# Performance work log

Hardware: AMD Instinct MI355X
Metric: run time of the kernel (lower is better)

## Reference

```python
import jax, jax.numpy as jnp
import numpy as np

N_NODES = 50000
N_EDGES = 800000
F_IN = 128
HID = 64
N_LAYERS = 3
N_GRAPHS = 64
N_CLASS = 2


def setup_inputs() -> dict:
    key = jax.random.key(0)
    ks = jax.random.split(key, 8)
    x = jax.random.normal(ks[0], (N_NODES, F_IN), jnp.float32)
    edge_index = jax.random.randint(ks[1], (2, N_EDGES), 0, N_NODES, dtype=jnp.int32)
    # sorted, balanced graph assignment so every graph id appears (max-pool safe)
    batch = (jnp.arange(N_NODES, dtype=jnp.int32) * N_GRAPHS) // N_NODES

    def lin(k, fi, fo):
        return jax.random.normal(k, (fi, fo), jnp.float32) / np.sqrt(fi).astype(np.float32)

    W1 = lin(ks[2], F_IN, HID)
    W2 = lin(ks[3], HID, HID)
    W3 = lin(ks[4], HID, HID)
    lin1_W = lin(ks[5], 3 * N_LAYERS * HID, HID)
    lin2_W = lin(ks[6], HID, N_CLASS)
    return dict(
        x=x,
        W1=W1, b1=jnp.zeros((HID,), jnp.float32),
        W2=W2, b2=jnp.zeros((HID,), jnp.float32),
        W3=W3, b3=jnp.zeros((HID,), jnp.float32),
        lin1_W=lin1_W, lin1_b=jnp.zeros((HID,), jnp.float32),
        lin2_W=lin2_W, lin2_b=jnp.zeros((N_CLASS,), jnp.float32),
        edge_index=edge_index, batch=batch,
    )


def reference(x, W1, b1, W2, b2, W3, b3, lin1_W, lin1_b, lin2_W, lin2_b,
              edge_index, batch):
    src, dst = edge_index[0], edge_index[1]
    # GCN symmetric normalization with self-loops (computed once, shared by layers)
    deg = jax.ops.segment_sum(jnp.ones((N_EDGES,), jnp.float32), dst, N_NODES) + 1.0
    dinv = jax.lax.rsqrt(deg)                      # [N]
    enorm = dinv[src] * dinv[dst]                  # [E]
    self_norm = (dinv * dinv)[:, None]             # [N,1] self-loop coeff

    def gcn_conv(h, W, b):
        h = h @ W                                  # [N, HID]
        agg = jax.ops.segment_sum(h[src] * enorm[:, None], dst, N_NODES)
        return agg + self_norm * h + b

    h = jax.nn.relu(gcn_conv(x, W1, b1))
    xs = [h]
    for W, b in ((W2, b2), (W3, b3)):
        h = jax.nn.relu(gcn_conv(h, W, b))
        xs.append(h)
    hcat = jnp.concatenate(xs, axis=1)             # JK 'cat': [N, 3*HID]

    add = jax.ops.segment_sum(hcat, batch, N_GRAPHS)
    cnt = jax.ops.segment_sum(jnp.ones((N_NODES,), jnp.float32), batch, N_GRAPHS)
    mean = add / cnt[:, None]
    mx = jax.ops.segment_max(hcat, batch, N_GRAPHS)
    g = jnp.concatenate([add, mean, mx], axis=1)   # [G, 9*HID]

    g = jax.nn.relu(g @ lin1_W + lin1_b)
    # dropout p=0.5 is identity in eval mode
    logits = g @ lin2_W + lin2_b
    return jax.nn.log_softmax(logits, axis=-1)
```

## Files before the change

### kernel.cpp

```cpp
#include <hip/hip_runtime.h>
#include <hip/hip_fp16.h>

#define N_NODES 50000
#define N_EDGES 800000
#define F_IN 128
#define HID 64
#define N_GRAPHS 64

#define SCAN_B ((N_NODES + 255) / 256)
#define FUSE_B ((N_EDGES + 255) / 256)

typedef _Float16 half8 __attribute__((ext_vector_type(8)));
typedef float f32x4 __attribute__((ext_vector_type(4)));

__global__ void deg_kernel(const int* __restrict__ ei, int* __restrict__ ideg, int E) {
    int i = blockIdx.x * blockDim.x + threadIdx.x;
    if (i * 4 >= E) return;
    int4 d = ((const int4*)(ei + E))[i];
    atomicAdd(&ideg[d.x], 1);
    atomicAdd(&ideg[d.y], 1);
    atomicAdd(&ideg[d.z], 1);
    atomicAdd(&ideg[d.w], 1);
}

__global__ void scan_part(const int* __restrict__ ideg, int* __restrict__ bsum, int n) {
    __shared__ int s[256];
    int t = threadIdx.x;
    int i = blockIdx.x * 256 + t;
    s[t] = (i < n) ? ideg[i] : 0;
    __syncthreads();
    for (int o = 128; o > 0; o >>= 1) {
        if (t < o) s[t] += s[t + o];
        __syncthreads();
    }
    if (t == 0) bsum[blockIdx.x] = s[0];
}

__global__ void scan_base(const int* __restrict__ bsum, int* __restrict__ bbase, int B) {
    __shared__ int s[256];
    int t = threadIdx.x;
    s[t] = (t < B) ? bsum[t] : 0;
    __syncthreads();
    for (int o = 1; o < 256; o <<= 1) {
        int v = (t >= o) ? s[t - o] : 0;
        __syncthreads();
        s[t] += v;
        __syncthreads();
    }
    if (t < B) bbase[t] = (t == 0) ? 0 : s[t - 1];
}

__global__ void scan_final(const int* __restrict__ ideg, const int* __restrict__ bbase,
                           int* __restrict__ offs, int* __restrict__ cur,
                           float* __restrict__ dinv, int n) {
    __shared__ int s[256];
    int t = threadIdx.x;
    int i = blockIdx.x * 256 + t;
    int v = (i < n) ? ideg[i] : 0;
    s[t] = v;
    __syncthreads();
    for (int o = 1; o < 256; o <<= 1) {
        int u = (t >= o) ? s[t - o] : 0;
        __syncthreads();
        s[t] += u;
        __syncthreads();
    }
    int excl = bbase[blockIdx.x] + s[t] - v;
    if (i < n) {
        offs[i] = excl; cur[i] = excl;
        dinv[i] = rsqrtf((float)v + 1.0f);
    }
    if (i == n - 1) offs[n] = excl + v;
}

__global__ void pack_weights(const float* __restrict__ W1, const float* __restrict__ W2,
                             const float* __restrict__ W3,
                             __half* __restrict__ W1t, __half* __restrict__ W2t,
                             __half* __restrict__ W3t) {
    int i = blockIdx.x * 256 + threadIdx.x;
    if (i < 8192) {
        int f = i >> 7, k = i & 127;
        W1t[i] = __float2half(W1[k * 64 + f]);
    } else if (i < 12288) {
        int j = i - 8192;
        int f = j >> 6, k = j & 63;
        W2t[j] = __float2half(W2[k * 64 + f]);
    } else if (i < 16384) {
        int l = i - 12288;
        int f = l >> 6, k = l & 63;
        W3t[l] = __float2half(W3[k * 64 + f]);
    }
}

__global__ __launch_bounds__(256) void fused_fill_mm1(
        const int* __restrict__ ei, const float* __restrict__ dinv,
        int* __restrict__ cur, unsigned int* __restrict__ csr,
        const float* __restrict__ X, const __half* __restrict__ W1t,
        __half* __restrict__ Y16, int E) {
    constexpr int SX = 136;
    __shared__ __half sXh[16 * SX];
    int tid = threadIdx.x;

    int e = blockIdx.x * 256 + tid;
    int esrc = ei[e];
    int d = ei[E + e];
    __half hw = __float2half(dinv[esrc]);
    unsigned int pk = ((unsigned int)(*(unsigned short*)&hw) << 16)
                    | (unsigned int)(esrc & 0xFFFF);
    int pos = atomicAdd(&cur[d], 1);

    int lane = tid & 63;
    int r = lane & 15, h = lane >> 4;
    int w = tid >> 6;
    const half8* Brow = (const half8*)(W1t + (size_t)(w * 16 + r) * F_IN + h * 8);
    half8 b0 = Brow[0];
    half8 b1 = Brow[4];
    half8 b2 = Brow[8];
    half8 b3 = Brow[12];

    int nodeBase = blockIdx.x * 16;
#pragma unroll
    for (int p = tid; p < 512; p += 256) {
        int row = p >> 5, c4 = p & 31;
        float4 v = *(const float4*)(X + (size_t)(nodeBase + row) * F_IN + c4 * 4);
        __half2 ab = __floats2half2_rn(v.x, v.y);
        __half2 cd = __floats2half2_rn(v.z, v.w);
        uint2 u; u.x = *(unsigned int*)&ab; u.y = *(unsigned int*)&cd;
        *(uint2*)&sXh[row * SX + c4 * 4] = u;
    }
    __syncthreads();

    f32x4 acc = {0.f, 0.f, 0.f, 0.f};
    half8 a0 = *(const half8*)&sXh[r * SX +  0 + h * 8];
    half8 a1 = *(const half8*)&sXh[r * SX + 32 + h * 8];
    half8 a2 = *(const half8*)&sXh[r * SX + 64 + h * 8];
    half8 a3 = *(const half8*)&sXh[r * SX + 96 + h * 8];
    acc = __builtin_amdgcn_mfma_f32_16x16x32_f16(a0, b0, acc, 0, 0, 0);
    acc = __builtin_amdgcn_mfma_f32_16x16x32_f16(a1, b1, acc, 0, 0, 0);
    acc = __builtin_amdgcn_mfma_f32_16x16x32_f16(a2, b2, acc, 0, 0, 0);
    acc = __builtin_amdgcn_mfma_f32_16x16x32_f16(a3, b3, acc, 0, 0, 0);
    int nodeT = nodeBase + h * 4;
#pragma unroll
    for (int reg = 0; reg < 4; ++reg)
        Y16[(size_t)(nodeT + reg) * 64 + w * 16 + r] = __float2half(acc[reg]);

    csr[pos] = pk;
}

__global__ __launch_bounds__(256) void matmul64_h(
        const __half* __restrict__ X, const __half* __restrict__ Wt,
        __half* __restrict__ Y16, int n) {
    int tid = threadIdx.x;
    int nodeBase = blockIdx.x * 64;
    int lane = tid & 63;
    int r = lane & 15, h = lane >> 4;
    int w = tid >> 6;
    int rowA = nodeBase + w * 16 + r;
    const half8* Arow = (const half8*)(X + (size_t)rowA * 64 + h * 8);
    half8 a0 = Arow[0];
    half8 a1 = Arow[4];
#pragma unroll
    for (int ft = 0; ft < 4; ++ft) {
        const half8* Brow = (const half8*)(Wt + (size_t)(ft * 16 + r) * 64 + h * 8);
        half8 b0 = Brow[0];
        half8 b1 = Brow[4];
        f32x4 acc = {0.f, 0.f, 0.f, 0.f};
        acc = __builtin_amdgcn_mfma_f32_16x16x32_f16(a0, b0, acc, 0, 0, 0);
        acc = __builtin_amdgcn_mfma_f32_16x16x32_f16(a1, b1, acc, 0, 0, 0);
        int nodeT = nodeBase + w * 16 + h * 4;
#pragma unroll
        for (int reg = 0; reg < 4; ++reg) {
            int node = nodeT + reg;
            if (node < n) Y16[(size_t)node * 64 + ft * 16 + r] = __float2half(acc[reg]);
        }
    }
}

__global__ void agg_kernel(const __half* __restrict__ hp16, const float* __restrict__ dinv,
                           const int* __restrict__ offs, const unsigned int* __restrict__ csr,
                           const float* __restrict__ b, __half* __restrict__ hout, int n) {
    int node = blockIdx.x * 4 + (threadIdx.x >> 6);
    if (node >= n) return;
    int lane = threadIdx.x & 63;
    int g = lane >> 3;
    int sub = lane & 7;
    int beg = offs[node], end = offs[node + 1];

    float a0 = 0.f, a1 = 0.f, a2 = 0.f, a3 = 0.f;
    float a4 = 0.f, a5 = 0.f, a6 = 0.f, a7 = 0.f;
#pragma unroll 2
    for (int i = beg; i < end; i += 8) {
        int idx = i + g;
        unsigned int pk = csr[min(idx, end - 1)];
        int src = (int)(pk & 0xFFFFu);
        __half_raw hr; hr.x = (unsigned short)(pk >> 16);
        float w = (idx < end) ? __half2float(*(__half*)&hr) : 0.f;
        uint4 hv = *(const uint4*)(hp16 + (size_t)src * 64 + sub * 8);
        float2 f01 = __half22float2(*(const __half2*)&hv.x);
        float2 f23 = __half22float2(*(const __half2*)&hv.y);
        float2 f45 = __half22float2(*(const __half2*)&hv.z);
        float2 f67 = __half22float2(*(const __half2*)&hv.w);
        a0 += f01.x * w; a1 += f01.y * w; a2 += f23.x * w; a3 += f23.y * w;
        a4 += f45.x * w; a5 += f45.y * w; a6 += f67.x * w; a7 += f67.y * w;
    }
#pragma unroll
    for (int m = 8; m <= 32; m <<= 1) {
        a0 += __shfl_xor(a0, m); a1 += __shfl_xor(a1, m);
        a2 += __shfl_xor(a2, m); a3 += __shfl_xor(a3, m);
        a4 += __shfl_xor(a4, m); a5 += __shfl_xor(a5, m);
        a6 += __shfl_xor(a6, m); a7 += __shfl_xor(a7, m);
    }

    float dn = dinv[node];
    uint4 sv = *(const uint4*)(hp16 + (size_t)node * 64 + sub * 8);
    float2 s01 = __half22float2(*(const __half2*)&sv.x);
    float2 s23 = __half22float2(*(const __half2*)&sv.y);
    float2 s45 = __half22float2(*(const __half2*)&sv.z);
    float2 s67 = __half22float2(*(const __half2*)&sv.w);
    float4 bA = *(const float4*)(b + sub * 8);
    float4 bB = *(const float4*)(b + sub * 8 + 4);
    float dn2 = dn * dn;
    float4 rA, rB;
    rA.x = dn * a0 + dn2 * s01.x + bA.x;  rA.x = rA.x > 0.f ? rA.x : 0.f;
    rA.y = dn * a1 + dn2 * s01.y + bA.y;  rA.y = rA.y > 0.f ? rA.y : 0.f;
    rA.z = dn * a2 + dn2 * s23.x + bA.z;  rA.z = rA.z > 0.f ? rA.z : 0.f;
    rA.w = dn * a3 + dn2 * s23.y + bA.w;  rA.w = rA.w > 0.f ? rA.w : 0.f;
    rB.x = dn * a4 + dn2 * s45.x + bB.x;  rB.x = rB.x > 0.f ? rB.x : 0.f;
    rB.y = dn * a5 + dn2 * s45.y + bB.y;  rB.y = rB.y > 0.f ? rB.y : 0.f;
    rB.z = dn * a6 + dn2 * s67.x + bB.z;  rB.z = rB.z > 0.f ? rB.z : 0.f;
    rB.w = dn * a7 + dn2 * s67.y + bB.w;  rB.w = rB.w > 0.f ? rB.w : 0.f;
    if (g == 0) {
        __half2 p0 = __floats2half2_rn(rA.x, rA.y);
        __half2 p1 = __floats2half2_rn(rA.z, rA.w);
        __half2 p2 = __floats2half2_rn(rB.x, rB.y);
        __half2 p3 = __floats2half2_rn(rB.z, rB.w);
        uint4 st;
        st.x = *(unsigned int*)&p0; st.y = *(unsigned int*)&p1;
        st.z = *(unsigned int*)&p2; st.w = *(unsigned int*)&p3;
        *(uint4*)(hout + (size_t)node * 64 + sub * 8) = st;
    }
}

__global__ void pool_kernel(const __half* __restrict__ h1, const __half* __restrict__ h2,
                            const __half* __restrict__ h3, const int* __restrict__ batch,
                            float* __restrict__ padd, unsigned int* __restrict__ pmax,
                            int* __restrict__ pcnt, int n, int chunk) {
    int f = threadIdx.x;
    int start = blockIdx.x * chunk;
    int end = min(start + chunk, n);
    if (start >= end) return;
    const __half* src = (f < 64) ? h1 : ((f < 128) ? h2 : h3);
    int fo = f & 63;
    float sum = 0.0f, mx = 0.0f;
    int g = batch[start];
    int runStart = start;
    for (int node = start; node < end; ++node) {
        int bg = batch[node];
        if (bg != g) {
            unsafeAtomicAdd(&padd[g * 192 + f], sum);
            atomicMax(&pmax[g * 192 + f], __float_as_uint(mx));
            if (f == 0) atomicAdd(&pcnt[g], node - runStart);
            sum = 0.0f; mx = 0.0f; g = bg; runStart = node;
        }
        float v = __half2float(src[(size_t)node * 64 + fo]);
        sum += v;
        mx = fmaxf(mx, v);
    }
    unsafeAtomicAdd(&padd[g * 192 + f], sum);
    atomicMax(&pmax[g * 192 + f], __float_as_uint(mx));
    if (f == 0) atomicAdd(&pcnt[g], end - runStart);
}

__global__ void mlp_kernel(const float* __restrict__ padd, const unsigned int* __restrict__ pmax,
                           const int* __restrict__ pcnt,
                           const float* __restrict__ lin1_W, const float* __restrict__ lin1_b,
                           const float* __restrict__ lin2_W, const float* __restrict__ lin2_b,
                           float* __restrict__ out) {
    int g = blockIdx.x;
    int t = threadIdx.x;
    __shared__ float gv[576];
    __shared__ float hid[64];
    float cnt = (float)pcnt[g];
    for (int i = t; i < 192; i += 64) {
        float a = padd[g * 192 + i];
        gv[i] = a;
        gv[192 + i] = a / cnt;
        gv[384 + i] = __uint_as_float(pmax[g * 192 + i]);
    }
    __syncthreads();
    float acc = lin1_b[t];
#pragma unroll 8
    for (int k = 0; k < 576; ++k) acc += gv[k] * lin1_W[k * 64 + t];
    hid[t] = acc > 0.0f ? acc : 0.0f;
    __syncthreads();
    if (t == 0) {
        float l0 = lin2_b[0], l1 = lin2_b[1];
        for (int k = 0; k < 64; ++k) {
            l0 += hid[k] * lin2_W[k * 2 + 0];
            l1 += hid[k] * lin2_W[k * 2 + 1];
        }
        float m = fmaxf(l0, l1);
        float lse = m + logf(expf(l0 - m) + expf(l1 - m));
        out[g * 2 + 0] = l0 - lse;
        out[g * 2 + 1] = l1 - lse;
    }
}

extern "C" void kernel_launch(void* const* d_in, const int* in_sizes, int n_in,
                              void* d_out, int out_size, void* d_ws, size_t ws_size,
                              hipStream_t stream) {
    const float* x      = (const float*)d_in[0];
    const float* W1     = (const float*)d_in[1];
    const float* b1     = (const float*)d_in[2];
    const float* W2     = (const float*)d_in[3];
    const float* b2     = (const float*)d_in[4];
    const float* W3     = (const float*)d_in[5];
    const float* b3     = (const float*)d_in[6];
    const float* lin1_W = (const float*)d_in[7];
    const float* lin1_b = (const float*)d_in[8];
    const float* lin2_W = (const float*)d_in[9];
    const float* lin2_b = (const float*)d_in[10];
    const int*   ei     = (const int*)d_in[11];
    const int*   batch  = (const int*)d_in[12];
    float* out = (float*)d_out;

    char* ws = (char*)d_ws;
    size_t off = 0;
    auto alloc = [&](size_t bytes) {
        void* p = ws + off;
        off = (off + bytes + 255) & ~(size_t)255;
        return p;
    };
    int*   ideg    = (int*)  alloc(N_NODES * 4);
    float* dinv    = (float*)alloc(N_NODES * 4);
    int*   offs    = (int*)  alloc((N_NODES + 1) * 4);
    int*   cur     = (int*)  alloc(N_NODES * 4);
    int*   bsum    = (int*)  alloc(SCAN_B * 4);
    int*   bbase   = (int*)  alloc(SCAN_B * 4);
    unsigned int* csr = (unsigned int*)alloc((size_t)N_EDGES * 4);
    __half* P      = (__half*)alloc((size_t)N_NODES * 64 * 2);
    __half* h1     = (__half*)alloc((size_t)N_NODES * 64 * 2);
    __half* h2     = (__half*)alloc((size_t)N_NODES * 64 * 2);
    __half* h3     = (__half*)alloc((size_t)N_NODES * 64 * 2);
    __half* W1t    = (__half*)alloc(64 * 128 * 2);
    __half* W2t    = (__half*)alloc(64 * 64 * 2);
    __half* W3t    = (__half*)alloc(64 * 64 * 2);
    float* padd    = (float*)alloc(N_GRAPHS * 192 * 4);
    unsigned int* pmax = (unsigned int*)alloc(N_GRAPHS * 192 * 4);
    int*   pcnt    = (int*) alloc(N_GRAPHS * 4);

    hipMemsetAsync(ideg, 0, N_NODES * 4, stream);
    deg_kernel<<<(N_EDGES / 4 + 255) / 256, 256, 0, stream>>>(ei, ideg, N_EDGES);
    scan_part <<<SCAN_B, 256, 0, stream>>>(ideg, bsum, N_NODES);
    scan_base <<<1, 256, 0, stream>>>(bsum, bbase, SCAN_B);
    scan_final<<<SCAN_B, 256, 0, stream>>>(ideg, bbase, offs, cur, dinv, N_NODES);
    pack_weights<<<64, 256, 0, stream>>>(W1, W2, W3, W1t, W2t, W3t);

    const int mmGrid  = (N_NODES + 63) / 64;
    const int aggGrid = (N_NODES + 3) / 4;

    fused_fill_mm1<<<FUSE_B, 256, 0, stream>>>(ei, dinv, cur, csr, x, W1t, P, N_EDGES);
    agg_kernel<<<aggGrid, 256, 0, stream>>>(P, dinv, offs, csr, b1, h1, N_NODES);
    matmul64_h<<<mmGrid, 256, 0, stream>>>(h1, W2t, P, N_NODES);
    agg_kernel<<<aggGrid, 256, 0, stream>>>(P, dinv, offs, csr, b2, h2, N_NODES);
    matmul64_h<<<mmGrid, 256, 0, stream>>>(h2, W3t, P, N_NODES);
    agg_kernel<<<aggGrid, 256, 0, stream>>>(P, dinv, offs, csr, b3, h3, N_NODES);

    hipMemsetAsync(padd, 0, N_GRAPHS * 192 * 4, stream);
    hipMemsetAsync(pmax, 0, N_GRAPHS * 192 * 4, stream);
    hipMemsetAsync(pcnt, 0, N_GRAPHS * 4, stream);
    const int chunk = (N_NODES + 511) / 512;
    pool_kernel<<<512, 192, 0, stream>>>(h1, h2, h3, batch, padd, pmax, pcnt, N_NODES, chunk);

    mlp_kernel<<<N_GRAPHS, 64, 0, stream>>>(padd, pmax, pcnt, lin1_W, lin1_b, lin2_W, lin2_b, out);
}
```

Measured before the change: 327.2 us.

## Fuse aggregation with next-layer matmul and graph pooling in one kernel

Merges the per-layer aggregation, the following 64x64 linear transform and the sum/max pooling into a single templated kernel. Each block stages its four output rows in shared memory, pools them with atomics (pre-reduced when all four nodes share a graph), then computes the next layer's projection with scalar FMAs instead of MFMA. This removes the separate matmul and pool kernels and the h1/h2/h3 intermediate buffers, and node counts now come from a small histogram kernel. In exchange it issues many more pooling atomics per layer and uses slower scalar arithmetic for the matmul, and it assumes N_NODES is a multiple of 4.

Result: slower. 396.7 us (+21.2%).

```diff
diff --git a/kernel.cpp b/kernel.cpp
--- a/kernel.cpp
+++ b/kernel.cpp
@@ -71,6 +71,17 @@
         dinv[i] = rsqrtf((float)v + 1.0f);
     }
     if (i == n - 1) offs[n] = excl + v;
+}
+
+__global__ void pcnt_kernel(const int* __restrict__ batch, int* __restrict__ pcnt, int n) {
+    __shared__ int hcnt[N_GRAPHS];
+    int t = threadIdx.x;
+    if (t < N_GRAPHS) hcnt[t] = 0;
+    __syncthreads();
+    int i = blockIdx.x * 256 + t;
+    if (i < n) atomicAdd(&hcnt[batch[i]], 1);
+    __syncthreads();
+    if (t < N_GRAPHS && hcnt[t]) atomicAdd(&pcnt[t], hcnt[t]);
 }
 
 __global__ void pack_weights(const float* __restrict__ W1, const float* __restrict__ W2,
@@ -147,41 +158,18 @@
     csr[pos] = pk;
 }
 
-__global__ __launch_bounds__(256) void matmul64_h(
-        const __half* __restrict__ X, const __half* __restrict__ Wt,
-        __half* __restrict__ Y16, int n) {
+template<int DO_MM>
+__global__ __launch_bounds__(256) void agg_fused(
+        const __half* __restrict__ Pin, const float* __restrict__ dinv,
+        const int* __restrict__ offs, const unsigned int* __restrict__ csr,
+        const float* __restrict__ b, const int* __restrict__ batch,
+        const __half* __restrict__ Wt, __half* __restrict__ Pout,
+        float* __restrict__ padd, unsigned int* __restrict__ pmax, int layerOff) {
+    __shared__ float hrow[4][64];
     int tid = threadIdx.x;
-    int nodeBase = blockIdx.x * 64;
+    int wid = tid >> 6;
+    int node = blockIdx.x * 4 + wid;
     int lane = tid & 63;
-    int r = lane & 15, h = lane >> 4;
-    int w = tid >> 6;
-    int rowA = nodeBase + w * 16 + r;
-    const half8* Arow = (const half8*)(X + (size_t)rowA * 64 + h * 8);
-    half8 a0 = Arow[0];
-    half8 a1 = Arow[4];
-#pragma unroll
-    for (int ft = 0; ft < 4; ++ft) {
-        const half8* Brow = (const half8*)(Wt + (size_t)(ft * 16 + r) * 64 + h * 8);
-        half8 b0 = Brow[0];
-        half8 b1 = Brow[4];
-        f32x4 acc = {0.f, 0.f, 0.f, 0.f};
-        acc = __builtin_amdgcn_mfma_f32_16x16x32_f16(a0, b0, acc, 0, 0, 0);
-        acc = __builtin_amdgcn_mfma_f32_16x16x32_f16(a1, b1, acc, 0, 0, 0);
-        int nodeT = nodeBase + w * 16 + h * 4;
-#pragma unroll
-        for (int reg = 0; reg < 4; ++reg) {
-            int node = nodeT + reg;
-            if (node < n) Y16[(size_t)node * 64 + ft * 16 + r] = __float2half(acc[reg]);
-        }
-    }
-}
-
-__global__ void agg_kernel(const __half* __restrict__ hp16, const float* __restrict__ dinv,
-                           const int* __restrict__ offs, const unsigned int* __restrict__ csr,
-                           const float* __restrict__ b, __half* __restrict__ hout, int n) {
-    int node = blockIdx.x * 4 + (threadIdx.x >> 6);
-    if (node >= n) return;
-    int lane = threadIdx.x & 63;
     int g = lane >> 3;
     int sub = lane & 7;
     int beg = offs[node], end = offs[node + 1];
@@ -195,7 +183,7 @@
         int src = (int)(pk & 0xFFFFu);
         __half_raw hr; hr.x = (unsigned short)(pk >> 16);
         float w = (idx < end) ? __half2float(*(__half*)&hr) : 0.f;
-        uint4 hv = *(const uint4*)(hp16 + (size_t)src * 64 + sub * 8);
+        uint4 hv = *(const uint4*)(Pin + (size_t)src * 64 + sub * 8);
         float2 f01 = __half22float2(*(const __half2*)&hv.x);
         float2 f23 = __half22float2(*(const __half2*)&hv.y);
         float2 f45 = __half22float2(*(const __half2*)&hv.z);
@@ -212,7 +200,7 @@
     }
 
     float dn = dinv[node];
-    uint4 sv = *(const uint4*)(hp16 + (size_t)node * 64 + sub * 8);
+    uint4 sv = *(const uint4*)(Pin + (size_t)node * 64 + sub * 8);
     float2 s01 = __half22float2(*(const __half2*)&sv.x);
     float2 s23 = __half22float2(*(const __half2*)&sv.y);
     float2 s45 = __half22float2(*(const __half2*)&sv.z);
@@ -230,45 +218,43 @@
     rB.z = dn * a6 + dn2 * s67.x + bB.z;  rB.z = rB.z > 0.f ? rB.z : 0.f;
     rB.w = dn * a7 + dn2 * s67.y + bB.w;  rB.w = rB.w > 0.f ? rB.w : 0.f;
     if (g == 0) {
-        __half2 p0 = __floats2half2_rn(rA.x, rA.y);
-        __half2 p1 = __floats2half2_rn(rA.z, rA.w);
-        __half2 p2 = __floats2half2_rn(rB.x, rB.y);
-        __half2 p3 = __floats2half2_rn(rB.z, rB.w);
-        uint4 st;
-        st.x = *(unsigned int*)&p0; st.y = *(unsigned int*)&p1;
-        st.z = *(unsigned int*)&p2; st.w = *(unsigned int*)&p3;
-        *(uint4*)(hout + (size_t)node * 64 + sub * 8) = st;
-    }
-}
-
-__global__ void pool_kernel(const __half* __restrict__ h1, const __half* __restrict__ h2,
-                            const __half* __restrict__ h3, const int* __restrict__ batch,
-                            float* __restrict__ padd, unsigned int* __restrict__ pmax,
-                            int* __restrict__ pcnt, int n, int chunk) {
-    int f = threadIdx.x;
-    int start = blockIdx.x * chunk;
-    int end = min(start + chunk, n);
-    if (start >= end) return;
-    const __half* src = (f < 64) ? h1 : ((f < 128) ? h2 : h3);
-    int fo = f & 63;
-    float sum = 0.0f, mx = 0.0f;
-    int g = batch[start];
-    int runStart = start;
-    for (int node = start; node < end; ++node) {
-        int bg = batch[node];
-        if (bg != g) {
-            unsafeAtomicAdd(&padd[g * 192 + f], sum);
-            atomicMax(&pmax[g * 192 + f], __float_as_uint(mx));
-            if (f == 0) atomicAdd(&pcnt[g], node - runStart);
-            sum = 0.0f; mx = 0.0f; g = bg; runStart = node;
+        *(float4*)&hrow[wid][sub * 8]     = rA;
+        *(float4*)&hrow[wid][sub * 8 + 4] = rB;
+    }
+    __syncthreads();
+
+    int nd = wid, f = lane;
+    int gb0 = batch[blockIdx.x * 4];
+    int gb3 = batch[blockIdx.x * 4 + 3];
+    if (gb0 == gb3) {
+        if (nd == 0) {
+            float s = hrow[0][f] + hrow[1][f] + hrow[2][f] + hrow[3][f];
+            float m = fmaxf(fmaxf(hrow[0][f], hrow[1][f]), fmaxf(hrow[2][f], hrow[3][f]));
+            unsafeAtomicAdd(&padd[gb0 * 192 + layerOff + f], s);
+            atomicMax(&pmax[gb0 * 192 + layerOff + f], __float_as_uint(m));
         }
-        float v = __half2float(src[(size_t)node * 64 + fo]);
-        sum += v;
-        mx = fmaxf(mx, v);
-    }
-    unsafeAtomicAdd(&padd[g * 192 + f], sum);
-    atomicMax(&pmax[g * 192 + f], __float_as_uint(mx));
-    if (f == 0) atomicAdd(&pcnt[g], end - runStart);
+    } else {
+        int gg = batch[node];
+        float v = hrow[nd][f];
+        unsafeAtomicAdd(&padd[gg * 192 + layerOff + f], v);
+        atomicMax(&pmax[gg * 192 + layerOff + f], __float_as_uint(v));
+    }
+
+    if constexpr (DO_MM) {
+        float acc = 0.f;
+        const float4* hr4 = (const float4*)hrow[nd];
+        const half8* wr = (const half8*)(Wt + (size_t)f * 64);
+#pragma unroll
+        for (int c = 0; c < 8; ++c) {
+            half8 w8 = wr[c];
+            float4 hA = hr4[c * 2], hB = hr4[c * 2 + 1];
+            acc += hA.x * (float)w8[0] + hA.y * (float)w8[1]
+                 + hA.z * (float)w8[2] + hA.w * (float)w8[3];
+            acc += hB.x * (float)w8[4] + hB.y * (float)w8[5]
+                 + hB.z * (float)w8[6] + hB.w * (float)w8[7];
+        }
+        Pout[(size_t)node * 64 + f] = __float2half(acc);
+    }
 }
 
 __global__ void mlp_kernel(const float* __restrict__ padd, const unsigned int* __restrict__ pmax,
@@ -338,10 +324,8 @@
     int*   bsum    = (int*)  alloc(SCAN_B * 4);
     int*   bbase   = (int*)  alloc(SCAN_B * 4);
     unsigned int* csr = (unsigned int*)alloc((size_t)N_EDGES * 4);
-    __half* P      = (__half*)alloc((size_t)N_NODES * 64 * 2);
-    __half* h1     = (__half*)alloc((size_t)N_NODES * 64 * 2);
-    __half* h2     = (__half*)alloc((size_t)N_NODES * 64 * 2);
-    __half* h3     = (__half*)alloc((size_t)N_NODES * 64 * 2);
+    __half* PA     = (__half*)alloc((size_t)N_NODES * 64 * 2);
+    __half* PB     = (__half*)alloc((size_t)N_NODES * 64 * 2);
     __half* W1t    = (__half*)alloc(64 * 128 * 2);
     __half* W2t    = (__half*)alloc(64 * 64 * 2);
     __half* W3t    = (__half*)alloc(64 * 64 * 2);
@@ -350,27 +334,26 @@
     int*   pcnt    = (int*) alloc(N_GRAPHS * 4);
 
     hipMemsetAsync(ideg, 0, N_NODES * 4, stream);
+    hipMemsetAsync(padd, 0, N_GRAPHS * 192 * 4, stream);
+    hipMemsetAsync(pmax, 0, N_GRAPHS * 192 * 4, stream);
+    hipMemsetAsync(pcnt, 0, N_GRAPHS * 4, stream);
+
     deg_kernel<<<(N_EDGES / 4 + 255) / 256, 256, 0, stream>>>(ei, ideg, N_EDGES);
     scan_part <<<SCAN_B, 256, 0, stream>>>(ideg, bsum, N_NODES);
     scan_base <<<1, 256, 0, stream>>>(bsum, bbase, SCAN_B);
     scan_final<<<SCAN_B, 256, 0, stream>>>(ideg, bbase, offs, cur, dinv, N_NODES);
     pack_weights<<<64, 256, 0, stream>>>(W1, W2, W3, W1t, W2t, W3t);
-
-    const int mmGrid  = (N_NODES + 63) / 64;
-    const int aggGrid = (N_NODES + 3) / 4;
-
-    fused_fill_mm1<<<FUSE_B, 256, 0, stream>>>(ei, dinv, cur, csr, x, W1t, P, N_EDGES);
-    agg_kernel<<<aggGrid, 256, 0, stream>>>(P, dinv, offs, csr, b1, h1, N_NODES);
-    matmul64_h<<<mmGrid, 256, 0, stream>>>(h1, W2t, P, N_NODES);
-    agg_kernel<<<aggGrid, 256, 0, stream>>>(P, dinv, offs, csr, b2, h2, N_NODES);
-    matmul64_h<<<mmGrid, 256, 0, stream>>>(h2, W3t, P, N_NODES);
-    agg_kernel<<<aggGrid, 256, 0, stream>>>(P, dinv, offs, csr, b3, h3, N_NODES);
-
-    hipMemsetAsync(padd, 0, N_GRAPHS * 192 * 4, stream);
-    hipMemsetAsync(pmax, 0, N_GRAPHS * 192 * 4, stream);
-    hipMemsetAsync(pcnt, 0, N_GRAPHS * 4, stream);
-    const int chunk = (N_NODES + 511) / 512;
-    pool_kernel<<<512, 192, 0, stream>>>(h1, h2, h3, batch, padd, pmax, pcnt, N_NODES, chunk);
+    pcnt_kernel<<<SCAN_B, 256, 0, stream>>>(batch, pcnt, N_NODES);
+
+    const int aggGrid = N_NODES / 4;
+
+    fused_fill_mm1<<<FUSE_B, 256, 0, stream>>>(ei, dinv, cur, csr, x, W1t, PA, N_EDGES);
+    agg_fused<1><<<aggGrid, 256, 0, stream>>>(PA, dinv, offs, csr, b1, batch, W2t, PB,
+                                              padd, pmax, 0);
+    agg_fused<1><<<aggGrid, 256, 0, stream>>>(PB, dinv, offs, csr, b2, batch, W3t, PA,
+                                              padd, pmax, 64);
+    agg_fused<0><<<aggGrid, 256, 0, stream>>>(PA, dinv, offs, csr, b3, batch, nullptr, nullptr,
+                                              padd, pmax, 128);
 
     mlp_kernel<<<N_GRAPHS, 64, 0, stream>>>(padd, pmax, pcnt, lin1_W, lin1_b, lin2_W, lin2_b, out);
 }
```
